# Kernel optimization log

Measured on AMD Instinct MI355X. Metric: run time of the kernel, lower is better.

The kernel has to match this reference:

```python
import jax, jax.numpy as jnp
import numpy as np

DIM = 768
HEADS = 12
DIM_HEAD = 64
ROPE_BASE = 8192.0
LN_EPS = 1e-5


def setup_inputs() -> dict:
    key = jax.random.key(0)
    k1, k2, k3, k4 = jax.random.split(key, 4)
    B, N = 4, 2048
    x = jax.random.normal(k1, (B, N, DIM), dtype=jnp.float32)
    # 2D (time, pitch) coordinates in [0, 64)
    coords = jax.random.uniform(k2, (B, N, 2), dtype=jnp.float32) * 64.0
    ln_gamma = jnp.ones((DIM,), dtype=jnp.float32)
    ln_beta = jnp.zeros((DIM,), dtype=jnp.float32)
    w_qkv = jax.random.normal(k3, (3 * HEADS * DIM_HEAD, DIM), dtype=jnp.float32) * (DIM ** -0.5)
    w_out = jax.random.normal(k4, (DIM, HEADS * DIM_HEAD), dtype=jnp.float32) * ((HEADS * DIM_HEAD) ** -0.5)
    return {"x": x, "coords": coords, "ln_gamma": ln_gamma, "ln_beta": ln_beta,
            "w_qkv": w_qkv, "w_out": w_out}


def _rotate(t, cos, sin):
    # t: [B,H,N,ad]; cos/sin: [B,1,N,ad//2]
    t1 = t[..., 0::2]
    t2 = t[..., 1::2]
    return jnp.concatenate([t1 * cos - t2 * sin, t1 * sin + t2 * cos], axis=-1)


def _axis_cos_sin(coord, axis_dim):
    # coord: [B,N] -> cos/sin: [B,1,N,axis_dim//2]
    half = axis_dim // 2
    exp = jnp.arange(half, dtype=jnp.float32) / half
    inv_freq = jnp.exp(-exp * jnp.log(jnp.float32(ROPE_BASE)))  # [half]
    freqs = coord[:, :, None] * inv_freq[None, None, :]  # [B,N,half]
    return jnp.cos(freqs)[:, None], jnp.sin(freqs)[:, None]


def reference(x, coords, ln_gamma, ln_beta, w_qkv, w_out):
    B, N, D = x.shape
    scale = DIM_HEAD ** -0.5

    # LayerNorm
    mu = jnp.mean(x, axis=-1, keepdims=True)
    var = jnp.mean((x - mu) ** 2, axis=-1, keepdims=True)
    xn = (x - mu) * jax.lax.rsqrt(var + LN_EPS) * ln_gamma + ln_beta

    # QKV projection: [B,N,3*H*dh]
    qkv = jnp.einsum('bnd,ed->bne', xn, w_qkv)
    q, k, v = jnp.split(qkv, 3, axis=-1)

    def to_heads(t):
        return t.reshape(B, N, HEADS, DIM_HEAD).transpose(0, 2, 1, 3)  # b h n d
    q, k, v = to_heads(q), to_heads(k), to_heads(v)

    # 2D axial RoPE: x-axis on dims [0:dh//2), y-axis on dims [dh//2:dh)
    half = DIM_HEAD // 2
    slices = [(0, (0, half)), (1, (half, DIM_HEAD))]
    for axis_idx, (lo, hi) in slices:
        cos, sin = _axis_cos_sin(coords[..., axis_idx], hi - lo)
        q = jnp.concatenate([q[..., :lo], _rotate(q[..., lo:hi], cos, sin), q[..., hi:]], axis=-1)
        k = jnp.concatenate([k[..., :lo], _rotate(k[..., lo:hi], cos, sin), k[..., hi:]], axis=-1)

    # Attention
    dots = jnp.einsum('bhnd,bhmd->bhnm', q, k) * scale
    attn = jax.nn.softmax(dots, axis=-1)
    out = jnp.einsum('bhnm,bhmd->bhnd', attn, v)
    out = out.transpose(0, 2, 1, 3).reshape(B, N, HEADS * DIM_HEAD)
    return jnp.einsum('bne,de->bnd', out, w_out)
```

## Files before the change

### kernel.cpp

```cpp
#include <hip/hip_runtime.h>

#define B_ 4
#define N_ 2048
#define D_ 768
#define H_ 12
#define DH_ 64
#define ROWS_ (B_*N_)
#define E3_ (3*D_)

typedef _Float16 f16;
typedef __attribute__((ext_vector_type(8))) _Float16 half8;
typedef __attribute__((ext_vector_type(4))) _Float16 half4;
typedef __attribute__((ext_vector_type(2))) _Float16 half2;
typedef __attribute__((ext_vector_type(4))) float floatx4;

__device__ __forceinline__ void gload_lds16(const void* g, void* lds){
  __builtin_amdgcn_global_load_lds(
      (const __attribute__((address_space(1))) unsigned int*)g,
      (__attribute__((address_space(3))) unsigned int*)lds, 16, 0, 0);
}

__global__ __launch_bounds__(256) void cvt_kernel(const float* __restrict__ srcA,
    f16* __restrict__ dstA, int n8a, const float* __restrict__ srcB,
    f16* __restrict__ dstB, int n8b){
  int i = blockIdx.x*256 + threadIdx.x;
  const float* src; f16* dst; int j;
  if (i < n8a){ src = srcA; dst = dstA; j = i; }
  else { j = i - n8a; if (j >= n8b) return; src = srcB; dst = dstB; }
  float4 a = ((const float4*)src)[2*j];
  float4 b = ((const float4*)src)[2*j+1];
  half8 h;
  h[0]=(f16)a.x; h[1]=(f16)a.y; h[2]=(f16)a.z; h[3]=(f16)a.w;
  h[4]=(f16)b.x; h[5]=(f16)b.y; h[6]=(f16)b.z; h[7]=(f16)b.w;
  *(half8*)(dst + (size_t)j*8) = h;
}

__global__ __launch_bounds__(256) void ln_kernel(const float* __restrict__ x,
    const float* __restrict__ g, const float* __restrict__ be, f16* __restrict__ xn){
  int w = threadIdx.x >> 6, lane = threadIdx.x & 63;
  int row = blockIdx.x*4 + w;
  const float* xr = x + (size_t)row * D_;
  int c = lane*4;
  float4 f0 = *(const float4*)(xr + c);
  float4 f1 = *(const float4*)(xr + c + 256);
  float4 f2 = *(const float4*)(xr + c + 512);
  float s  = (f0.x+f0.y+f0.z+f0.w) + (f1.x+f1.y+f1.z+f1.w) + (f2.x+f2.y+f2.z+f2.w);
  float ss = (f0.x*f0.x+f0.y*f0.y+f0.z*f0.z+f0.w*f0.w)
           + (f1.x*f1.x+f1.y*f1.y+f1.z*f1.z+f1.w*f1.w)
           + (f2.x*f2.x+f2.y*f2.y+f2.z*f2.z+f2.w*f2.w);
  #pragma unroll
  for(int off=1; off<64; off<<=1){
    s  += __shfl_xor(s,  off, 64);
    ss += __shfl_xor(ss, off, 64);
  }
  float mean = s * (1.0f/D_);
  float var  = ss * (1.0f/D_) - mean*mean;
  float rstd = rsqrtf(var + 1e-5f);
  f16* xo = xn + (size_t)row * D_;
  #pragma unroll
  for(int part=0; part<3; ++part){
    float4 v = part==0 ? f0 : (part==1 ? f1 : f2);
    float4 gg = *(const float4*)(g  + c + part*256);
    float4 bb = *(const float4*)(be + c + part*256);
    half4 o;
    o[0] = (f16)((v.x-mean)*rstd*gg.x + bb.x);
    o[1] = (f16)((v.y-mean)*rstd*gg.y + bb.y);
    o[2] = (f16)((v.z-mean)*rstd*gg.z + bb.z);
    o[3] = (f16)((v.w-mean)*rstd*gg.w + bb.w);
    *(half4*)(xo + c + part*256) = o;
  }
}

__global__ __launch_bounds__(256) void rope_tab_kernel(const float* __restrict__ coords,
    float* __restrict__ T){
  int i = blockIdx.x*256 + threadIdx.x;
  int token = i >> 5, ax = (i >> 4) & 1, m = i & 15;
  float coord = coords[(size_t)token*2 + ax];
  float fr = exp2f((float)m * (-13.0f/16.0f));
  float sn, cs;
  sincosf(coord * fr, &sn, &cs);
  T[(size_t)token*64 + ax*32 + m]      = cs;
  T[(size_t)token*64 + ax*32 + 16 + m] = sn;
}

__global__ __launch_bounds__(256) void qkv_gemm(const f16* __restrict__ A,
    const f16* __restrict__ W, const float* __restrict__ T,
    f16* __restrict__ Q, f16* __restrict__ Kt, f16* __restrict__ VT){
  __shared__ __align__(16) char smem[128*136*2];
  f16* sA = (f16*)smem;
  f16* sB = (f16*)(smem + 8192);
  f16* sT = (f16*)smem;
  int tid = threadIdx.x;
  int w = tid >> 6, lane = tid & 63, quad = lane >> 4, l15 = lane & 15;
  int row0 = blockIdx.y * 128;
  int e0   = blockIdx.x * 128;
  int wr = (w >> 1) * 64, wc = (w & 1) * 64;
  int r0c = tid >> 2,        ci0 = (tid & 3) * 8;
  int r1c = (256+tid) >> 2,  ci1 = (tid & 3) * 8;
  floatx4 acc[4][4];
  #pragma unroll
  for(int i=0;i<4;++i)
    #pragma unroll
    for(int j=0;j<4;++j) acc[i][j] = (floatx4){0.f,0.f,0.f,0.f};

  for(int k0=0; k0<D_; k0+=32){
    __syncthreads();
    gload_lds16(A + (size_t)(row0+r0c)*D_ + k0 + ci0, sA + (size_t)(w*64)*8);
    gload_lds16(A + (size_t)(row0+r1c)*D_ + k0 + ci1, sA + (size_t)(256 + w*64)*8);
    gload_lds16(W + (size_t)(e0 +r0c)*D_ + k0 + ci0, sB + (size_t)(w*64)*8);
    gload_lds16(W + (size_t)(e0 +r1c)*D_ + k0 + ci1, sB + (size_t)(256 + w*64)*8);
    __syncthreads();
    half8 af[4], bf[4];
    #pragma unroll
    for(int mi=0;mi<4;++mi) af[mi] = *(const half8*)&sA[(wr + mi*16 + l15)*32 + quad*8];
    #pragma unroll
    for(int ni=0;ni<4;++ni) bf[ni] = *(const half8*)&sB[(wc + ni*16 + l15)*32 + quad*8];
    #pragma unroll
    for(int mi=0;mi<4;++mi)
      #pragma unroll
      for(int ni=0;ni<4;++ni)
        acc[mi][ni] = __builtin_amdgcn_mfma_f32_16x16x32_f16(af[mi], bf[ni], acc[mi][ni], 0, 0, 0);
  }
  int part = e0 / D_;
  int erel = e0 % D_;
  if (part == 2){
    #pragma unroll
    for(int ni=0;ni<4;++ni){
      int col = erel + wc + ni*16 + l15;
      int h = col >> 6, d = col & 63;
      #pragma unroll
      for(int mi=0;mi<4;++mi){
        int rbase = row0 + wr + mi*16 + quad*4;
        int b = rbase >> 11, n = rbase & 2047;
        half4 h4;
        #pragma unroll
        for(int reg=0;reg<4;++reg) h4[reg] = (f16)acc[mi][ni][reg];
        *(half4*)&VT[(((size_t)b*H_ + h)*DH_ + d)*N_ + n] = h4;
      }
    }
    return;
  }
  __syncthreads();
  #pragma unroll
  for(int mi=0;mi<4;++mi){
    int r = wr + mi*16 + quad*4;
    #pragma unroll
    for(int ni=0;ni<4;++ni){
      int c = wc + ni*16 + l15;
      #pragma unroll
      for(int reg=0;reg<4;++reg)
        sT[(size_t)(r+reg)*136 + c] = (f16)acc[mi][ni][reg];
    }
  }
  __syncthreads();
  int r  = tid >> 1;
  int hh = tid & 1;
  int n_global = row0 + r;
  const float* tt = T + (size_t)n_global*64;
  float tv[64];
  #pragma unroll
  for(int j=0;j<16;++j) *(float4*)&tv[j*4] = *(const float4*)(tt + j*4);
  f16 v[64];
  #pragma unroll
  for(int j=0;j<8;++j) *(half8*)&v[j*8] = *(const half8*)&sT[(size_t)r*136 + hh*64 + j*8];
  f16 o[64];
  #pragma unroll
  for(int ax=0; ax<2; ++ax){
    #pragma unroll
    for(int m=0;m<16;++m){
      float cs = tv[ax*32 + m];
      float sn = tv[ax*32 + 16 + m];
      float t1 = (float)v[ax*32 + 2*m];
      float t2 = (float)v[ax*32 + 2*m + 1];
      o[ax*32 + m]      = (f16)(t1*cs - t2*sn);
      o[ax*32 + 16 + m] = (f16)(t1*sn + t2*cs);
    }
  }
  int h = erel/64 + hh;
  int b = n_global >> 11, n = n_global & 2047;
  f16* dst = (part==0) ? Q : Kt;
  f16* op = dst + (((size_t)b*H_ + h)*N_ + n)*DH_;
  #pragma unroll
  for(int j=0;j<8;++j) *(half8*)(op + j*8) = *(half8*)&o[j*8];
}

__global__ __launch_bounds__(256, 3) void attn_kernel(const f16* __restrict__ Q,
    const f16* __restrict__ K, const f16* __restrict__ VT, f16* __restrict__ AO){
  __shared__ f16 sK[2][64*64];
  __shared__ f16 sV[2][64*64];
  __shared__ f16 sP[4][2][16*64];
  int bh = blockIdx.y;
  int q0 = blockIdx.x * 128;
  int tid = threadIdx.x;
  int w = tid >> 6, lane = tid & 63, quad = lane >> 4, l15 = lane & 15;
  const f16* Qb = Q  + (size_t)bh*N_*DH_;
  const f16* Ks = K  + (size_t)bh*N_*DH_;
  const f16* Vb = VT + (size_t)bh*DH_*N_;

  int sd = tid >> 2, sc = tid & 3;
  const f16* vp = Vb + (size_t)sd*N_ + sc*16;
  const f16* kp = Ks + (size_t)sd*DH_ + sc*16;
  int sw0 = sd*64 + (((2*sc    ) ^ (sd & 7)) << 3);
  int sw1 = sd*64 + (((2*sc + 1) ^ (sd & 7)) << 3);

  half8 qf0[2], qf1[2];
  #pragma unroll
  for(int s2=0;s2<2;++s2){
    const f16* qrow = Qb + (size_t)(q0 + 32*w + 16*s2 + l15)*DH_ + quad*8;
    qf0[s2] = *(const half8*)(qrow);
    qf1[s2] = *(const half8*)(qrow + 32);
    half8 cs8;
    #pragma unroll
    for(int j=0;j<8;++j) cs8[j] = (f16)0.18033688f;
    qf0[s2] = qf0[s2] * cs8;
    qf1[s2] = qf1[s2] * cs8;
  }

  {
    half8 k0 = *(const half8*)(kp);
    half8 k1 = *(const half8*)(kp + 8);
    half8 g0 = *(const half8*)(vp);
    half8 g1 = *(const half8*)(vp + 8);
    *(half8*)&sK[0][sw0] = k0;  *(half8*)&sK[0][sw1] = k1;
    *(half8*)&sV[0][sw0] = g0;  *(half8*)&sV[0][sw1] = g1;
  }
  kp += 64*DH_;  vp += 64;

  float l_run[2] = {0.0f, 0.0f};
  floatx4 acc[2][4];
  #pragma unroll
  for(int s2=0;s2<2;++s2)
    #pragma unroll
    for(int dt=0;dt<4;++dt) acc[s2][dt] = (floatx4){0.f,0.f,0.f,0.f};
  __syncthreads();

  int sw = l15 & 7;
  f16* Prow[2] = { &sP[w][0][l15*64], &sP[w][1][l15*64] };

  const floatx4 SINIT = (floatx4){-8.f,-8.f,-8.f,-8.f};

#define ATTN_BODY(CUR, NXT) { \
    half8 nk0 = *(const half8*)(kp);      half8 nk1 = *(const half8*)(kp + 8); \
    half8 ng0 = *(const half8*)(vp);      half8 ng1 = *(const half8*)(vp + 8); \
    kp += 64*DH_;  vp += 64; \
    const f16* sk = &sK[CUR][0]; \
    half8 kf0[4], kf1[4]; \
    _Pragma("unroll") \
    for(int nt=0;nt<4;++nt){ \
      int rr = 16*nt + l15; \
      kf0[nt] = *(const half8*)&sk[rr*64 + ((quad       ^ sw) << 3)]; \
      kf1[nt] = *(const half8*)&sk[rr*64 + (((quad + 4) ^ sw) << 3)]; \
    } \
    floatx4 s_[2][4]; \
    _Pragma("unroll") \
    for(int s2=0;s2<2;++s2) \
      _Pragma("unroll") \
      for(int nt=0; nt<4; ++nt){ \
        floatx4 z = SINIT; \
        z = __builtin_amdgcn_mfma_f32_16x16x32_f16(kf0[nt], qf0[s2], z, 0, 0, 0); \
        z = __builtin_amdgcn_mfma_f32_16x16x32_f16(kf1[nt], qf1[s2], z, 0, 0, 0); \
        s_[s2][nt] = z; \
      } \
    _Pragma("unroll") \
    for(int s2=0;s2<2;++s2){ \
      f16* Pb = Prow[s2]; \
      float r4[4]; \
      _Pragma("unroll") \
      for(int nt=0;nt<4;++nt){ \
        float p0 = __builtin_amdgcn_exp2f(s_[s2][nt][0]); \
        float p1 = __builtin_amdgcn_exp2f(s_[s2][nt][1]); \
        float p2 = __builtin_amdgcn_exp2f(s_[s2][nt][2]); \
        float p3 = __builtin_amdgcn_exp2f(s_[s2][nt][3]); \
        auto lo_ = __builtin_amdgcn_cvt_pkrtz(p0, p1); \
        auto hi_ = __builtin_amdgcn_cvt_pkrtz(p2, p3); \
        half2 lo, hi; \
        __builtin_memcpy(&lo, &lo_, 4);  __builtin_memcpy(&hi, &hi_, 4); \
        half4 h = __builtin_shufflevector(lo, hi, 0, 1, 2, 3); \
        *(half4*)&Pb[(((2*nt + (quad>>1)) ^ sw) << 3) + ((quad & 1) << 2)] = h; \
        r4[nt] = (p0+p1)+(p2+p3); \
      } \
      l_run[s2] += (r4[0]+r4[1])+(r4[2]+r4[3]); \
    } \
    { \
      const f16* sv = &sV[CUR][0]; \
      half8 pf0a = *(const half8*)&Prow[0][((quad       ^ sw) << 3)]; \
      half8 pf1a = *(const half8*)&Prow[0][(((4 + quad) ^ sw) << 3)]; \
      half8 pf0b = *(const half8*)&Prow[1][((quad       ^ sw) << 3)]; \
      half8 pf1b = *(const half8*)&Prow[1][(((4 + quad) ^ sw) << 3)]; \
      _Pragma("unroll") \
      for(int dt=0;dt<4;++dt){ \
        int rr = 16*dt + l15; \
        half8 v0 = *(const half8*)&sv[rr*64 + ((quad       ^ sw) << 3)]; \
        half8 v1 = *(const half8*)&sv[rr*64 + (((quad + 4) ^ sw) << 3)]; \
        acc[0][dt] = __builtin_amdgcn_mfma_f32_16x16x32_f16(v0, pf0a, acc[0][dt], 0, 0, 0); \
        acc[0][dt] = __builtin_amdgcn_mfma_f32_16x16x32_f16(v1, pf1a, acc[0][dt], 0, 0, 0); \
        acc[1][dt] = __builtin_amdgcn_mfma_f32_16x16x32_f16(v0, pf0b, acc[1][dt], 0, 0, 0); \
        acc[1][dt] = __builtin_amdgcn_mfma_f32_16x16x32_f16(v1, pf1b, acc[1][dt], 0, 0, 0); \
      } \
    } \
    { \
      f16* dk = &sK[NXT][0]; \
      f16* dv = &sV[NXT][0]; \
      *(half8*)&dk[sw0] = nk0;  *(half8*)&dk[sw1] = nk1; \
      *(half8*)&dv[sw0] = ng0;  *(half8*)&dv[sw1] = ng1; \
    } \
    __syncthreads(); \
  }

  #pragma unroll 1
  for(int t=0; t<N_/128; ++t){
    ATTN_BODY(0, 1);
    ATTN_BODY(1, 0);
  }
#undef ATTN_BODY

  int b = bh / H_, h = bh % H_;
  #pragma unroll
  for(int s2=0;s2<2;++s2){
    float l = l_run[s2];
    l += __shfl_xor(l, 16, 64);
    l += __shfl_xor(l, 32, 64);
    float inv = 1.0f / l;
    f16* Pb = Prow[s2];
    #pragma unroll
    for(int dt=0;dt<4;++dt){
      half4 h4;
      h4[0]=(f16)(acc[s2][dt][0]*inv); h4[1]=(f16)(acc[s2][dt][1]*inv);
      h4[2]=(f16)(acc[s2][dt][2]*inv); h4[3]=(f16)(acc[s2][dt][3]*inv);
      *(half4*)&Pb[(((2*dt + (quad>>1)) ^ sw) << 3) + ((quad & 1) << 2)] = h4;
    }
    half8 o0 = *(const half8*)&Pb[(((2*quad    ) ^ sw) << 3)];
    half8 o1 = *(const half8*)&Pb[(((2*quad + 1) ^ sw) << 3)];
    f16* op = AO + ((size_t)(b*N_ + q0 + 32*w + 16*s2 + l15))*D_ + h*DH_ + quad*16;
    *(half8*)(op)     = o0;
    *(half8*)(op + 8) = o1;
  }
}

__global__ __launch_bounds__(256) void out_gemm(const f16* __restrict__ A,
    const f16* __restrict__ W, float* __restrict__ C){
  __shared__ f16 sA[128*32];
  __shared__ f16 sB[128*32];
  int tid = threadIdx.x;
  int w = tid >> 6, lane = tid & 63, quad = lane >> 4, l15 = lane & 15;
  int row0 = blockIdx.y * 128;
  int e0   = blockIdx.x * 128;
  int wr = (w >> 1) * 64, wc = (w & 1) * 64;
  int r0c = tid >> 2,        ci0 = (tid & 3) * 8;
  int r1c = (256+tid) >> 2,  ci1 = (tid & 3) * 8;
  floatx4 acc[4][4];
  #pragma unroll
  for(int i=0;i<4;++i)
    #pragma unroll
    for(int j=0;j<4;++j) acc[i][j] = (floatx4){0.f,0.f,0.f,0.f};

  for(int k0=0; k0<D_; k0+=32){
    __syncthreads();
    gload_lds16(A + (size_t)(row0+r0c)*D_ + k0 + ci0, sA + (size_t)(w*64)*8);
    gload_lds16(A + (size_t)(row0+r1c)*D_ + k0 + ci1, sA + (size_t)(256 + w*64)*8);
    gload_lds16(W + (size_t)(e0 +r0c)*D_ + k0 + ci0, sB + (size_t)(w*64)*8);
    gload_lds16(W + (size_t)(e0 +r1c)*D_ + k0 + ci1, sB + (size_t)(256 + w*64)*8);
    __syncthreads();
    half8 af[4], bf[4];
    #pragma unroll
    for(int mi=0;mi<4;++mi) af[mi] = *(const half8*)&sA[(wr + mi*16 + l15)*32 + quad*8];
    #pragma unroll
    for(int ni=0;ni<4;++ni) bf[ni] = *(const half8*)&sB[(wc + ni*16 + l15)*32 + quad*8];
    #pragma unroll
    for(int mi=0;mi<4;++mi)
      #pragma unroll
      for(int ni=0;ni<4;++ni)
        acc[mi][ni] = __builtin_amdgcn_mfma_f32_16x16x32_f16(af[mi], bf[ni], acc[mi][ni], 0, 0, 0);
  }
  #pragma unroll
  for(int ni=0;ni<4;++ni){
    int col = e0 + wc + ni*16 + l15;
    #pragma unroll
    for(int mi=0;mi<4;++mi){
      int rbase = row0 + wr + mi*16 + quad*4;
      #pragma unroll
      for(int reg=0;reg<4;++reg)
        C[(size_t)(rbase+reg)*D_ + col] = acc[mi][ni][reg];
    }
  }
}

extern "C" void kernel_launch(void* const* d_in, const int* in_sizes, int n_in,
                              void* d_out, int out_size, void* d_ws, size_t ws_size,
                              hipStream_t stream) {
  (void)in_sizes; (void)n_in; (void)out_size; (void)ws_size;
  const float* x      = (const float*)d_in[0];
  const float* coords = (const float*)d_in[1];
  const float* g      = (const float*)d_in[2];
  const float* be     = (const float*)d_in[3];
  const float* wqkv   = (const float*)d_in[4];
  const float* wout   = (const float*)d_in[5];
  float* out = (float*)d_out;
  char* ws = (char*)d_ws;
  const size_t SEG = (size_t)ROWS_ * D_ * 2;
  f16* xn  = (f16*)(ws + 0*SEG);
  f16* Q   = (f16*)(ws + 1*SEG);
  f16* K   = (f16*)(ws + 2*SEG);
  f16* VT  = (f16*)(ws + 3*SEG);
  f16* AO  = (f16*)(ws + 4*SEG);
  f16* W16 = (f16*)(ws + 5*SEG);
  f16* Wo16= (f16*)(ws + 5*SEG + (size_t)E3_*D_*2);
  float* T = (float*)AO;

  const int n8a = E3_*D_/8, n8b = D_*D_/8;
  cvt_kernel <<<(n8a+n8b+255)/256, 256, 0, stream>>>(wqkv, W16, n8a, wout, Wo16, n8b);
  ln_kernel  <<<ROWS_/4, 256, 0, stream>>>(x, g, be, xn);
  rope_tab_kernel<<<(B_*N_*32)/256, 256, 0, stream>>>(coords, T);
  qkv_gemm   <<<dim3(E3_/128, ROWS_/128), 256, 0, stream>>>(xn, W16, T, Q, K, VT);
  attn_kernel<<<dim3(N_/128, B_*H_), 256, 0, stream>>>(Q, K, VT, AO);
  out_gemm   <<<dim3(D_/128, ROWS_/128), 256, 0, stream>>>(AO, Wo16, out);
}
```

Measured before the change: 242.8 us.

## Use direct global-to-LDS loads with XOR swizzle in attention and GEMMs

The attention kernel now streams K and V tiles straight into LDS with global_load_lds instead of staging them through registers. The loads are source-side swizzled, so LDS stays bank-conflict free for the fragment reads. The QKV and output GEMMs double their K-step to 64 with the same swizzled layout, halving the number of barriers and fixing bank conflicts on the A/B fragment reads. This costs more LDS per GEMM block and relies on async LDS writes finishing before the barrier.

```diff
diff --git a/kernel.cpp b/kernel.cpp
--- a/kernel.cpp
+++ b/kernel.cpp
@@ -88,38 +88,46 @@
     f16* __restrict__ Q, f16* __restrict__ Kt, f16* __restrict__ VT){
   __shared__ __align__(16) char smem[128*136*2];
   f16* sA = (f16*)smem;
-  f16* sB = (f16*)(smem + 8192);
+  f16* sB = (f16*)(smem + 16384);
   f16* sT = (f16*)smem;
   int tid = threadIdx.x;
   int w = tid >> 6, lane = tid & 63, quad = lane >> 4, l15 = lane & 15;
   int row0 = blockIdx.y * 128;
   int e0   = blockIdx.x * 128;
   int wr = (w >> 1) * 64, wc = (w & 1) * 64;
-  int r0c = tid >> 2,        ci0 = (tid & 3) * 8;
-  int r1c = (256+tid) >> 2,  ci1 = (tid & 3) * 8;
+  int r8 = lane >> 3;
+  int sc16 = ((lane & 7) ^ r8) * 8;
+  int sw = l15 & 7;
   floatx4 acc[4][4];
   #pragma unroll
   for(int i=0;i<4;++i)
     #pragma unroll
     for(int j=0;j<4;++j) acc[i][j] = (floatx4){0.f,0.f,0.f,0.f};
 
-  for(int k0=0; k0<D_; k0+=32){
+  for(int k0=0; k0<D_; k0+=64){
     __syncthreads();
-    gload_lds16(A + (size_t)(row0+r0c)*D_ + k0 + ci0, sA + (size_t)(w*64)*8);
-    gload_lds16(A + (size_t)(row0+r1c)*D_ + k0 + ci1, sA + (size_t)(256 + w*64)*8);
-    gload_lds16(W + (size_t)(e0 +r0c)*D_ + k0 + ci0, sB + (size_t)(w*64)*8);
-    gload_lds16(W + (size_t)(e0 +r1c)*D_ + k0 + ci1, sB + (size_t)(256 + w*64)*8);
+    #pragma unroll
+    for(int j=0;j<4;++j){
+      int rr = j*32 + w*8 + r8;
+      gload_lds16(A + (size_t)(row0+rr)*D_ + k0 + sc16, sA + (j*32 + w*8)*64);
+      gload_lds16(W + (size_t)(e0 +rr)*D_ + k0 + sc16, sB + (j*32 + w*8)*64);
+    }
     __syncthreads();
-    half8 af[4], bf[4];
-    #pragma unroll
-    for(int mi=0;mi<4;++mi) af[mi] = *(const half8*)&sA[(wr + mi*16 + l15)*32 + quad*8];
-    #pragma unroll
-    for(int ni=0;ni<4;++ni) bf[ni] = *(const half8*)&sB[(wc + ni*16 + l15)*32 + quad*8];
-    #pragma unroll
-    for(int mi=0;mi<4;++mi)
+    #pragma unroll
+    for(int kk=0;kk<2;++kk){
+      half8 af[4], bf[4];
+      #pragma unroll
+      for(int mi=0;mi<4;++mi)
+        af[mi] = *(const half8*)&sA[(wr + mi*16 + l15)*64 + (((kk*4 + quad) ^ sw) << 3)];
       #pragma unroll
       for(int ni=0;ni<4;++ni)
-        acc[mi][ni] = __builtin_amdgcn_mfma_f32_16x16x32_f16(af[mi], bf[ni], acc[mi][ni], 0, 0, 0);
+        bf[ni] = *(const half8*)&sB[(wc + ni*16 + l15)*64 + (((kk*4 + quad) ^ sw) << 3)];
+      #pragma unroll
+      for(int mi=0;mi<4;++mi)
+        #pragma unroll
+        for(int ni=0;ni<4;++ni)
+          acc[mi][ni] = __builtin_amdgcn_mfma_f32_16x16x32_f16(af[mi], bf[ni], acc[mi][ni], 0, 0, 0);
+    }
   }
   int part = e0 / D_;
   int erel = e0 % D_;
@@ -197,11 +205,12 @@
   const f16* Ks = K  + (size_t)bh*N_*DH_;
   const f16* Vb = VT + (size_t)bh*DH_*N_;
 
-  int sd = tid >> 2, sc = tid & 3;
-  const f16* vp = Vb + (size_t)sd*N_ + sc*16;
-  const f16* kp = Ks + (size_t)sd*DH_ + sc*16;
-  int sw0 = sd*64 + (((2*sc    ) ^ (sd & 7)) << 3);
-  int sw1 = sd*64 + (((2*sc + 1) ^ (sd & 7)) << 3);
+  int r8 = lane >> 3;
+  int swsrc = ((lane & 7) ^ r8) * 8;
+  const f16* kst0 = Ks + (size_t)(w*16 +     r8)*DH_ + swsrc;
+  const f16* kst1 = Ks + (size_t)(w*16 + 8 + r8)*DH_ + swsrc;
+  const f16* vst0 = Vb + (size_t)(w*16 +     r8)*N_  + swsrc;
+  const f16* vst1 = Vb + (size_t)(w*16 + 8 + r8)*N_  + swsrc;
 
   half8 qf0[2], qf1[2];
   #pragma unroll
@@ -216,15 +225,11 @@
     qf1[s2] = qf1[s2] * cs8;
   }
 
-  {
-    half8 k0 = *(const half8*)(kp);
-    half8 k1 = *(const half8*)(kp + 8);
-    half8 g0 = *(const half8*)(vp);
-    half8 g1 = *(const half8*)(vp + 8);
-    *(half8*)&sK[0][sw0] = k0;  *(half8*)&sK[0][sw1] = k1;
-    *(half8*)&sV[0][sw0] = g0;  *(half8*)&sV[0][sw1] = g1;
-  }
-  kp += 64*DH_;  vp += 64;
+  gload_lds16(kst0, &sK[0][(w*16    )*64]);
+  gload_lds16(kst1, &sK[0][(w*16 + 8)*64]);
+  gload_lds16(vst0, &sV[0][(w*16    )*64]);
+  gload_lds16(vst1, &sV[0][(w*16 + 8)*64]);
+  kst0 += 64*DH_; kst1 += 64*DH_; vst0 += 64; vst1 += 64;
 
   float l_run[2] = {0.0f, 0.0f};
   floatx4 acc[2][4];
@@ -240,9 +245,11 @@
   const floatx4 SINIT = (floatx4){-8.f,-8.f,-8.f,-8.f};
 
 #define ATTN_BODY(CUR, NXT) { \
-    half8 nk0 = *(const half8*)(kp);      half8 nk1 = *(const half8*)(kp + 8); \
-    half8 ng0 = *(const half8*)(vp);      half8 ng1 = *(const half8*)(vp + 8); \
-    kp += 64*DH_;  vp += 64; \
+    gload_lds16(kst0, &sK[NXT][(w*16    )*64]); \
+    gload_lds16(kst1, &sK[NXT][(w*16 + 8)*64]); \
+    gload_lds16(vst0, &sV[NXT][(w*16    )*64]); \
+    gload_lds16(vst1, &sV[NXT][(w*16 + 8)*64]); \
+    kst0 += 64*DH_; kst1 += 64*DH_; vst0 += 64; vst1 += 64; \
     const f16* sk = &sK[CUR][0]; \
     half8 kf0[4], kf1[4]; \
     _Pragma("unroll") \
@@ -298,12 +305,6 @@
         acc[1][dt] = __builtin_amdgcn_mfma_f32_16x16x32_f16(v1, pf1b, acc[1][dt], 0, 0, 0); \
       } \
     } \
-    { \
-      f16* dk = &sK[NXT][0]; \
-      f16* dv = &sV[NXT][0]; \
-      *(half8*)&dk[sw0] = nk0;  *(half8*)&dk[sw1] = nk1; \
-      *(half8*)&dv[sw0] = ng0;  *(half8*)&dv[sw1] = ng1; \
-    } \
     __syncthreads(); \
   }
 
@@ -339,38 +340,46 @@
 
 __global__ __launch_bounds__(256) void out_gemm(const f16* __restrict__ A,
     const f16* __restrict__ W, float* __restrict__ C){
-  __shared__ f16 sA[128*32];
-  __shared__ f16 sB[128*32];
+  __shared__ f16 sA[128*64];
+  __shared__ f16 sB[128*64];
   int tid = threadIdx.x;
   int w = tid >> 6, lane = tid & 63, quad = lane >> 4, l15 = lane & 15;
   int row0 = blockIdx.y * 128;
   int e0   = blockIdx.x * 128;
   int wr = (w >> 1) * 64, wc = (w & 1) * 64;
-  int r0c = tid >> 2,        ci0 = (tid & 3) * 8;
-  int r1c = (256+tid) >> 2,  ci1 = (tid & 3) * 8;
+  int r8 = lane >> 3;
+  int sc16 = ((lane & 7) ^ r8) * 8;
+  int sw = l15 & 7;
   floatx4 acc[4][4];
   #pragma unroll
   for(int i=0;i<4;++i)
     #pragma unroll
     for(int j=0;j<4;++j) acc[i][j] = (floatx4){0.f,0.f,0.f,0.f};
 
-  for(int k0=0; k0<D_; k0+=32){
+  for(int k0=0; k0<D_; k0+=64){
     __syncthreads();
-    gload_lds16(A + (size_t)(row0+r0c)*D_ + k0 + ci0, sA + (size_t)(w*64)*8);
-    gload_lds16(A + (size_t)(row0+r1c)*D_ + k0 + ci1, sA + (size_t)(256 + w*64)*8);
-    gload_lds16(W + (size_t)(e0 +r0c)*D_ + k0 + ci0, sB + (size_t)(w*64)*8);
-    gload_lds16(W + (size_t)(e0 +r1c)*D_ + k0 + ci1, sB + (size_t)(256 + w*64)*8);
+    #pragma unroll
+    for(int j=0;j<4;++j){
+      int rr = j*32 + w*8 + r8;
+      gload_lds16(A + (size_t)(row0+rr)*D_ + k0 + sc16, sA + (j*32 + w*8)*64);
+      gload_lds16(W + (size_t)(e0 +rr)*D_ + k0 + sc16, sB + (j*32 + w*8)*64);
+    }
     __syncthreads();
-    half8 af[4], bf[4];
-    #pragma unroll
-    for(int mi=0;mi<4;++mi) af[mi] = *(const half8*)&sA[(wr + mi*16 + l15)*32 + quad*8];
-    #pragma unroll
-    for(int ni=0;ni<4;++ni) bf[ni] = *(const half8*)&sB[(wc + ni*16 + l15)*32 + quad*8];
-    #pragma unroll
-    for(int mi=0;mi<4;++mi)
+    #pragma unroll
+    for(int kk=0;kk<2;++kk){
+      half8 af[4], bf[4];
+      #pragma unroll
+      for(int mi=0;mi<4;++mi)
+        af[mi] = *(const half8*)&sA[(wr + mi*16 + l15)*64 + (((kk*4 + quad) ^ sw) << 3)];
       #pragma unroll
       for(int ni=0;ni<4;++ni)
-        acc[mi][ni] = __builtin_amdgcn_mfma_f32_16x16x32_f16(af[mi], bf[ni], acc[mi][ni], 0, 0, 0);
+        bf[ni] = *(const half8*)&sB[(wc + ni*16 + l15)*64 + (((kk*4 + quad) ^ sw) << 3)];
+      #pragma unroll
+      for(int mi=0;mi<4;++mi)
+        #pragma unroll
+        for(int ni=0;ni<4;++ni)
+          acc[mi][ni] = __builtin_amdgcn_mfma_f32_16x16x32_f16(af[mi], bf[ni], acc[mi][ni], 0, 0, 0);
+    }
   }
   #pragma unroll
   for(int ni=0;ni<4;++ni){
```

Result: slower. 275.8 us (+13.6%).

## Double-buffer LDS in QKV and output GEMMs; raise wave priority around attention MFMAs

Applied to the files above, without the earlier changes.

Both projection GEMMs now use two LDS buffers, issuing the async global-to-LDS load for the next K slice before computing on the current one. This removes one barrier per step and overlaps memory latency with MFMA work. The attention inner loop wraps its MFMA blocks in s_setprio so matrix work is scheduled ahead of other waves. LDS use per GEMM block doubles, which may reduce occupancy. Correctness relies on the global_load_lds writes being complete at the barrier without an explicit vmcnt wait.

```diff
diff --git a/kernel.cpp b/kernel.cpp
--- a/kernel.cpp
+++ b/kernel.cpp
@@ -86,10 +86,10 @@
 __global__ __launch_bounds__(256) void qkv_gemm(const f16* __restrict__ A,
     const f16* __restrict__ W, const float* __restrict__ T,
     f16* __restrict__ Q, f16* __restrict__ Kt, f16* __restrict__ VT){
-  __shared__ __align__(16) char smem[128*136*2];
-  f16* sA = (f16*)smem;
-  f16* sB = (f16*)(smem + 8192);
-  f16* sT = (f16*)smem;
+  __shared__ __align__(16) char smem[34816];
+  f16* sA0 = (f16*)smem;            f16* sA1 = (f16*)(smem + 8192);
+  f16* sB0 = (f16*)(smem + 16384);  f16* sB1 = (f16*)(smem + 24576);
+  f16* sT  = (f16*)smem;
   int tid = threadIdx.x;
   int w = tid >> 6, lane = tid & 63, quad = lane >> 4, l15 = lane & 15;
   int row0 = blockIdx.y * 128;
@@ -103,24 +103,41 @@
     #pragma unroll
     for(int j=0;j<4;++j) acc[i][j] = (floatx4){0.f,0.f,0.f,0.f};
 
-  for(int k0=0; k0<D_; k0+=32){
+#define GEMM_STAGE(dA, dB, kk) { \
+    gload_lds16(A + (size_t)(row0+r0c)*D_ + (kk) + ci0, (dA) + (w*64)*8); \
+    gload_lds16(A + (size_t)(row0+r1c)*D_ + (kk) + ci1, (dA) + (256 + w*64)*8); \
+    gload_lds16(W + (size_t)(e0 +r0c)*D_ + (kk) + ci0, (dB) + (w*64)*8); \
+    gload_lds16(W + (size_t)(e0 +r1c)*D_ + (kk) + ci1, (dB) + (256 + w*64)*8); }
+
+#define GEMM_COMPUTE(pA, pB) { \
+    half8 af[4], bf[4]; \
+    _Pragma("unroll") \
+    for(int mi=0;mi<4;++mi) af[mi] = *(const half8*)&(pA)[(wr + mi*16 + l15)*32 + quad*8]; \
+    _Pragma("unroll") \
+    for(int ni=0;ni<4;++ni) bf[ni] = *(const half8*)&(pB)[(wc + ni*16 + l15)*32 + quad*8]; \
+    _Pragma("unroll") \
+    for(int mi=0;mi<4;++mi) \
+      _Pragma("unroll") \
+      for(int ni=0;ni<4;++ni) \
+        acc[mi][ni] = __builtin_amdgcn_mfma_f32_16x16x32_f16(af[mi], bf[ni], acc[mi][ni], 0, 0, 0); }
+
+  GEMM_STAGE(sA0, sB0, 0);
+  __syncthreads();
+  #pragma unroll 1
+  for(int t=0; t<11; ++t){
+    int k0 = t*64;
+    GEMM_STAGE(sA1, sB1, k0+32);
+    GEMM_COMPUTE(sA0, sB0);
     __syncthreads();
-    gload_lds16(A + (size_t)(row0+r0c)*D_ + k0 + ci0, sA + (size_t)(w*64)*8);
-    gload_lds16(A + (size_t)(row0+r1c)*D_ + k0 + ci1, sA + (size_t)(256 + w*64)*8);
-    gload_lds16(W + (size_t)(e0 +r0c)*D_ + k0 + ci0, sB + (size_t)(w*64)*8);
-    gload_lds16(W + (size_t)(e0 +r1c)*D_ + k0 + ci1, sB + (size_t)(256 + w*64)*8);
+    GEMM_STAGE(sA0, sB0, k0+64);
+    GEMM_COMPUTE(sA1, sB1);
     __syncthreads();
-    half8 af[4], bf[4];
-    #pragma unroll
-    for(int mi=0;mi<4;++mi) af[mi] = *(const half8*)&sA[(wr + mi*16 + l15)*32 + quad*8];
-    #pragma unroll
-    for(int ni=0;ni<4;++ni) bf[ni] = *(const half8*)&sB[(wc + ni*16 + l15)*32 + quad*8];
-    #pragma unroll
-    for(int mi=0;mi<4;++mi)
-      #pragma unroll
-      for(int ni=0;ni<4;++ni)
-        acc[mi][ni] = __builtin_amdgcn_mfma_f32_16x16x32_f16(af[mi], bf[ni], acc[mi][ni], 0, 0, 0);
-  }
+  }
+  GEMM_STAGE(sA1, sB1, 736);
+  GEMM_COMPUTE(sA0, sB0);
+  __syncthreads();
+  GEMM_COMPUTE(sA1, sB1);
+
   int part = e0 / D_;
   int erel = e0 % D_;
   if (part == 2){
@@ -252,6 +269,7 @@
       kf1[nt] = *(const half8*)&sk[rr*64 + (((quad + 4) ^ sw) << 3)]; \
     } \
     floatx4 s_[2][4]; \
+    __builtin_amdgcn_s_setprio(1); \
     _Pragma("unroll") \
     for(int s2=0;s2<2;++s2) \
       _Pragma("unroll") \
@@ -261,6 +279,7 @@
         z = __builtin_amdgcn_mfma_f32_16x16x32_f16(kf1[nt], qf1[s2], z, 0, 0, 0); \
         s_[s2][nt] = z; \
       } \
+    __builtin_amdgcn_s_setprio(0); \
     _Pragma("unroll") \
     for(int s2=0;s2<2;++s2){ \
       f16* Pb = Prow[s2]; \
@@ -287,6 +306,7 @@
       half8 pf1a = *(const half8*)&Prow[0][(((4 + quad) ^ sw) << 3)]; \
       half8 pf0b = *(const half8*)&Prow[1][((quad       ^ sw) << 3)]; \
       half8 pf1b = *(const half8*)&Prow[1][(((4 + quad) ^ sw) << 3)]; \
+      __builtin_amdgcn_s_setprio(1); \
       _Pragma("unroll") \
       for(int dt=0;dt<4;++dt){ \
         int rr = 16*dt + l15; \
@@ -297,6 +317,7 @@
         acc[1][dt] = __builtin_amdgcn_mfma_f32_16x16x32_f16(v0, pf0b, acc[1][dt], 0, 0, 0); \
         acc[1][dt] = __builtin_amdgcn_mfma_f32_16x16x32_f16(v1, pf1b, acc[1][dt], 0, 0, 0); \
       } \
+      __builtin_amdgcn_s_setprio(0); \
     } \
     { \
       f16* dk = &sK[NXT][0]; \
@@ -339,8 +360,9 @@
 
 __global__ __launch_bounds__(256) void out_gemm(const f16* __restrict__ A,
     const f16* __restrict__ W, float* __restrict__ C){
-  __shared__ f16 sA[128*32];
-  __shared__ f16 sB[128*32];
+  __shared__ __align__(16) char smem[32768];
+  f16* sA0 = (f16*)smem;            f16* sA1 = (f16*)(smem + 8192);
+  f16* sB0 = (f16*)(smem + 16384);  f16* sB1 = (f16*)(smem + 24576);
   int tid = threadIdx.x;
   int w = tid >> 6, lane = tid & 63, quad = lane >> 4, l15 = lane & 15;
   int row0 = blockIdx.y * 128;
@@ -354,24 +376,23 @@
     #pragma unroll
     for(int j=0;j<4;++j) acc[i][j] = (floatx4){0.f,0.f,0.f,0.f};
 
-  for(int k0=0; k0<D_; k0+=32){
+  GEMM_STAGE(sA0, sB0, 0);
+  __syncthreads();
+  #pragma unroll 1
+  for(int t=0; t<11; ++t){
+    int k0 = t*64;
+    GEMM_STAGE(sA1, sB1, k0+32);
+    GEMM_COMPUTE(sA0, sB0);
     __syncthreads();
-    gload_lds16(A + (size_t)(row0+r0c)*D_ + k0 + ci0, sA + (size_t)(w*64)*8);
-    gload_lds16(A + (size_t)(row0+r1c)*D_ + k0 + ci1, sA + (size_t)(256 + w*64)*8);
-    gload_lds16(W + (size_t)(e0 +r0c)*D_ + k0 + ci0, sB + (size_t)(w*64)*8);
-    gload_lds16(W + (size_t)(e0 +r1c)*D_ + k0 + ci1, sB + (size_t)(256 + w*64)*8);
+    GEMM_STAGE(sA0, sB0, k0+64);
+    GEMM_COMPUTE(sA1, sB1);
     __syncthreads();
-    half8 af[4], bf[4];
-    #pragma unroll
-    for(int mi=0;mi<4;++mi) af[mi] = *(const half8*)&sA[(wr + mi*16 + l15)*32 + quad*8];
-    #pragma unroll
-    for(int ni=0;ni<4;++ni) bf[ni] = *(const half8*)&sB[(wc + ni*16 + l15)*32 + quad*8];
-    #pragma unroll
-    for(int mi=0;mi<4;++mi)
-      #pragma unroll
-      for(int ni=0;ni<4;++ni)
-        acc[mi][ni] = __builtin_amdgcn_mfma_f32_16x16x32_f16(af[mi], bf[ni], acc[mi][ni], 0, 0, 0);
-  }
+  }
+  GEMM_STAGE(sA1, sB1, 736);
+  GEMM_COMPUTE(sA0, sB0);
+  __syncthreads();
+  GEMM_COMPUTE(sA1, sB1);
+
   #pragma unroll
   for(int ni=0;ni<4;++ni){
     int col = e0 + wc + ni*16 + l15;
```

Result: slower. 411.3 us (+69.4%).
